# Kernel tuning notes

Measured on AMD Instinct MI355X. Metric: run time of the kernel, lower is better.

Reference implementation:

```python
import jax, jax.numpy as jnp
import numpy as np

EMB = 768
HEADS = 12
B, N = 32, 1024


def setup_inputs() -> dict:
    key = jax.random.key(0)
    ks = jax.random.split(key, 7)
    s = 1.0 / np.sqrt(EMB)
    return {
        "x": jax.random.normal(ks[0], (B, N, EMB), dtype=jnp.float32),
        "Wq": jax.random.normal(ks[1], (EMB, EMB), dtype=jnp.float32) * s,
        "bq": jnp.zeros((EMB,), dtype=jnp.float32),
        "Wk": jax.random.normal(ks[2], (EMB, EMB), dtype=jnp.float32) * s,
        "bk": jnp.zeros((EMB,), dtype=jnp.float32),
        "Wv": jax.random.normal(ks[3], (EMB, EMB), dtype=jnp.float32) * s,
        "bv": jnp.zeros((EMB,), dtype=jnp.float32),
    }


def reference(x, Wq, bq, Wk, bk, Wv, bv):
    b, n, _ = x.shape
    h = HEADS
    e = EMB // h  # head dim
    # project and split heads: b n (h e) -> b h n e
    def split(t):
        return t.reshape(b, n, h, e).transpose(0, 2, 1, 3)
    q = split(x @ Wq + bq)
    k = split(x @ Wk + bk)
    v = split(x @ Wv + bv)
    # NOTE: scale is 1/sqrt(num_head), as in the original module
    wei = jnp.einsum('bhie,bhje->bhij', q, k) / jnp.sqrt(jnp.float32(h))
    # NOTE: softmax over dim=2 = query axis i (non-standard)
    wei = jax.nn.softmax(wei, axis=2)
    # dropout is identity in eval mode
    out = jnp.einsum('bhij,bhje->bhie', wei, v)
    return out.transpose(0, 2, 1, 3).reshape(b, n, h * e)
```

## Files before the change

### kernel.cpp

```cpp
#include <hip/hip_runtime.h>

#define EMB 768
#define NH 12
#define HD 64
#define BB 32
#define NN 1024
#define QSCALE 0.41647025f

typedef _Float16 h8 __attribute__((ext_vector_type(8)));
typedef _Float16 h4 __attribute__((ext_vector_type(4)));
typedef _Float16 h2 __attribute__((ext_vector_type(2)));
typedef float f4 __attribute__((ext_vector_type(4)));

static __device__ __forceinline__ f4 mfma16(h8 a, h8 b, f4 c) {
  return __builtin_amdgcn_mfma_f32_16x16x32_f16(a, b, c, 0, 0, 0);
}

static __device__ __forceinline__ h2 cvt_pk(float a, float b) {
  return __builtin_bit_cast(h2, __builtin_amdgcn_cvt_pkrtz(a, b));
}

static __device__ __forceinline__ float exp2a(float x) {
#if __has_builtin(__builtin_amdgcn_exp2f)
  return __builtin_amdgcn_exp2f(x);
#else
  float r;
  asm("v_exp_f32 %0, %1\n\ts_nop 1" : "=v"(r) : "v"(x));
  return r;
#endif
}

static __device__ __forceinline__ void gload16(const _Float16* g, _Float16* lds) {
  __builtin_amdgcn_global_load_lds(
      (const __attribute__((address_space(1))) void*)g,
      (__attribute__((address_space(3))) void*)lds, 16, 0, 0);
}

__global__ __launch_bounds__(256) void k_cvt(const float* __restrict__ X,
                                             _Float16* __restrict__ Xh, int n4) {
  int i = blockIdx.x * 256 + threadIdx.x;
  if (i >= n4) return;
  float4 v = ((const float4*)X)[i];
  h4 o = {(_Float16)v.x, (_Float16)v.y, (_Float16)v.z, (_Float16)v.w};
  ((h4*)Xh)[i] = o;
}

__global__ __launch_bounds__(256) void k_wt(const float* __restrict__ W0,
                                            const float* __restrict__ W1,
                                            const float* __restrict__ W2,
                                            _Float16* __restrict__ Wt) {
  const float* W = blockIdx.z == 0 ? W0 : (blockIdx.z == 1 ? W1 : W2);
  _Float16* dst = Wt + (size_t)blockIdx.z * EMB * EMB;
  __shared__ float tile[64][65];
  const int t = threadIdx.x;
  const int r0 = blockIdx.y * 64, c0 = blockIdx.x * 64;
  const int r = t >> 4, c4 = (t & 15) * 4;
#pragma unroll
  for (int i = 0; i < 4; ++i) {
    const float4 v = *(const float4*)&W[(size_t)(r0 + r + 16 * i) * EMB + c0 + c4];
    tile[r + 16 * i][c4 + 0] = v.x; tile[r + 16 * i][c4 + 1] = v.y;
    tile[r + 16 * i][c4 + 2] = v.z; tile[r + 16 * i][c4 + 3] = v.w;
  }
  __syncthreads();
  const int cc = t >> 2, rr = (t & 3) * 16;
#pragma unroll
  for (int half = 0; half < 2; ++half) {
    h8 o;
#pragma unroll
    for (int j = 0; j < 8; ++j) o[j] = (_Float16)tile[rr + half * 8 + j][cc];
    *(h8*)&dst[(size_t)(c0 + cc) * EMB + r0 + rr + half * 8] = o;
  }
}

__global__ __launch_bounds__(256) void k_projf(const _Float16* __restrict__ Xh,
                                               const _Float16* __restrict__ Wt,
                                               const float* __restrict__ bq,
                                               const float* __restrict__ bk,
                                               const float* __restrict__ bv,
                                               _Float16* __restrict__ Qw,
                                               _Float16* __restrict__ Kw,
                                               _Float16* __restrict__ Vtmp) {
  __shared__ _Float16 As[2][128 * 64];
  __shared__ _Float16 Bs[2][128 * 64];
  const int t = threadIdx.x;
  const int w = t >> 6, l = t & 63;
  const int wm = w >> 1, wn = w & 1;
  const int p = l & 15, g = l >> 4;
  const int by = blockIdx.x;
  const int m0 = blockIdx.y * 128;
  const int n0 = by * 128;

  f4 acc[4][4];
#pragma unroll
  for (int mf = 0; mf < 4; ++mf)
#pragma unroll
    for (int nf = 0; nf < 4; ++nf) acc[mf][nf] = f4{0.f, 0.f, 0.f, 0.f};

  const int lrow = l >> 3, lch = (l & 7) ^ (l >> 3);

#define STAGE(buf, k0)                                                            \
  {                                                                               \
    _Float16* ab = &As[buf][0];                                                   \
    _Float16* bb = &Bs[buf][0];                                                   \
    _Pragma("unroll") for (int i = 0; i < 4; ++i) {                               \
      const int seg = (w << 2) | i;                                               \
      const int grow = (seg << 3) | lrow;                                         \
      gload16(Xh + (size_t)(m0 + grow) * EMB + (k0) + lch * 8, ab + seg * 512);   \
      gload16(Wt + (size_t)(n0 + grow) * EMB + (k0) + lch * 8, bb + seg * 512);   \
    }                                                                             \
  }

  STAGE(0, 0)
  __syncthreads();

  int cur = 0;
  for (int kt = 0; kt < 12; ++kt) {
    if (kt + 1 < 12) STAGE(cur ^ 1, (kt + 1) * 64)
    const char* asb = (const char*)&As[cur][0];
    const char* bsb = (const char*)&Bs[cur][0];
#pragma unroll
    for (int ks = 0; ks < 2; ++ks) {
      h8 af[4], bf[4];
#pragma unroll
      for (int mf = 0; mf < 4; ++mf)
        af[mf] = *(const h8*)(asb + ((wm * 64 + mf * 16 + p) << 7) +
                              ((((ks << 2) | g) ^ (p & 7)) << 4));
#pragma unroll
      for (int nf = 0; nf < 4; ++nf)
        bf[nf] = *(const h8*)(bsb + ((wn * 64 + nf * 16 + p) << 7) +
                              ((((ks << 2) | g) ^ (p & 7)) << 4));
#pragma unroll
      for (int mf = 0; mf < 4; ++mf)
#pragma unroll
        for (int nf = 0; nf < 4; ++nf) acc[mf][nf] = mfma16(af[mf], bf[nf], acc[mf][nf]);
    }
    __syncthreads();
    cur ^= 1;
  }
#undef STAGE

  const int z = by / 6;
  const int nl0 = (by % 6) * 128;
  const float* bias = z == 0 ? bq : (z == 1 ? bk : bv);
  _Float16* Outz = z == 0 ? Qw : (z == 1 ? Kw : Vtmp);
  const float scale = z == 0 ? QSCALE : 1.0f;
#pragma unroll
  for (int nf = 0; nf < 4; ++nf) {
    const int C = nl0 + wn * 64 + nf * 16 + p;
    const float bvv = bias[C];
    const int h = C >> 6, e = C & 63;
#pragma unroll
    for (int mf = 0; mf < 4; ++mf) {
#pragma unroll
      for (int r = 0; r < 4; ++r) {
        const int R = m0 + wm * 64 + mf * 16 + g * 4 + r;
        const int b = R >> 10, tok = R & 1023;
        Outz[((size_t)(b * NH + h) * NN + tok) * HD + e] = (_Float16)((acc[mf][nf][r] + bvv) * scale);
      }
    }
  }
}

__global__ __launch_bounds__(256) void k_stats(const _Float16* __restrict__ Q,
                                               const _Float16* __restrict__ K,
                                               const _Float16* __restrict__ Vtmp,
                                               float* __restrict__ MT,
                                               _Float16* __restrict__ Vt) {
  const int bh = blockIdx.x * 48 + (blockIdx.y >> 3);
  const int jt = blockIdx.y & 7;
  const int j0 = jt * 128;
  __shared__ __align__(16) char SMEM[35080];
  _Float16* Ks = (_Float16*)SMEM;
  _Float16* Qs = (_Float16*)(SMEM + 16384);
  float* Lj    = (float*)(SMEM + 32768);
  float* reds  = (float*)(SMEM + 33280);
  float* MsShp = (float*)(SMEM + 34312);
  _Float16 (*Vtile)[72] = (_Float16(*)[72])SMEM;
  const _Float16* Qb = Q + (size_t)bh * NN * HD;
  const _Float16* Kb = K + (size_t)bh * NN * HD;
  const int t = threadIdx.x, w = t >> 6, l = t & 63;
  const int wi = w >> 1, wj = w & 1;
  const int p = l & 15, g = l >> 4;
  const int lrow = l >> 3, lch = (l & 7) ^ (l >> 3);

#pragma unroll
  for (int i = 0; i < 4; ++i) {
    const int seg = (w << 2) | i;
    const int grow = (seg << 3) | lrow;
    gload16(Kb + (size_t)(j0 + grow) * HD + lch * 8, Ks + seg * 512);
  }
  if (t < 128) Lj[t] = 0.f;
  __syncthreads();

  const char* ksb = (const char*)Ks;
  const char* qsb = (const char*)Qs;
  for (int i0 = 0; i0 < NN; i0 += 128) {
#pragma unroll
    for (int i = 0; i < 4; ++i) {
      const int seg = (w << 2) | i;
      const int grow = (seg << 3) | lrow;
      gload16(Qb + (size_t)(i0 + grow) * HD + lch * 8, Qs + seg * 512);
    }
    __syncthreads();
    f4 s[4][4];
#pragma unroll
    for (int mf = 0; mf < 4; ++mf)
#pragma unroll
      for (int nf = 0; nf < 4; ++nf) s[mf][nf] = f4{0.f, 0.f, 0.f, 0.f};
#pragma unroll
    for (int ks = 0; ks < 2; ++ks) {
      h8 af[4], bf[4];
#pragma unroll
      for (int mf = 0; mf < 4; ++mf)
        af[mf] = *(const h8*)(qsb + ((wi * 64 + mf * 16 + p) << 7) + ((((ks << 2) | g) ^ (p & 7)) << 4));
#pragma unroll
      for (int nf = 0; nf < 4; ++nf)
        bf[nf] = *(const h8*)(ksb + ((wj * 64 + nf * 16 + p) << 7) + ((((ks << 2) | g) ^ (p & 7)) << 4));
#pragma unroll
      for (int mf = 0; mf < 4; ++mf)
#pragma unroll
        for (int nf = 0; nf < 4; ++nf) s[mf][nf] = mfma16(af[mf], bf[nf], s[mf][nf]);
    }
#pragma unroll
    for (int nf = 0; nf < 4; ++nf) {
      float cs = 0.f;
#pragma unroll
      for (int mf = 0; mf < 4; ++mf)
#pragma unroll
        for (int r = 0; r < 4; ++r) cs += exp2a(s[mf][nf][r]);
      cs += __shfl_xor(cs, 16);
      cs += __shfl_xor(cs, 32);
      if (l < 16) reds[wi * 128 + wj * 64 + nf * 16 + l] = cs;
    }
    __syncthreads();
    if (t < 128) Lj[t] += reds[t] + reds[128 + t];
    __syncthreads();
  }
  if (w == 0) {
    float mv = fmaxf(Lj[l], Lj[l + 64]);
#pragma unroll
    for (int d = 32; d; d >>= 1) mv = fmaxf(mv, __shfl_xor(mv, d));
    if (l == 0) { MsShp[0] = __log2f(mv); MT[bh * 8 + jt] = MsShp[0]; }
  }
  __syncthreads();
  const float rmsc = exp2a(MsShp[0]);

  const _Float16* Vb = Vtmp + (size_t)bh * NN * HD;
  _Float16* Vo = Vt + (size_t)bh * HD * NN;
  const int jr = t >> 3, c8 = (t & 7) * 8;
#pragma unroll
  for (int half = 0; half < 2; ++half) {
#pragma unroll
    for (int i = 0; i < 2; ++i) {
      const int jl = half * 64 + jr + 32 * i;
      const float inv = rmsc / Lj[jl];
      h8 v = *(const h8*)&Vb[(size_t)(j0 + jl) * HD + c8];
      h8 o;
#pragma unroll
      for (int j = 0; j < 8; ++j) o[j] = (_Float16)((float)v[j] * inv);
      *(h8*)&Vtile[jr + 32 * i][c8] = o;
    }
    __syncthreads();
#pragma unroll
    for (int i = 0; i < 2; ++i) {
      h8 o;
#pragma unroll
      for (int j = 0; j < 8; ++j) o[j] = Vtile[c8 + j][jr + 32 * i];
      *(h8*)&Vo[(size_t)(jr + 32 * i) * NN + j0 + half * 64 + c8] = o;
    }
    __syncthreads();
  }
}

__global__ __launch_bounds__(256) void k_out(const _Float16* __restrict__ Q,
                                             const _Float16* __restrict__ K,
                                             const _Float16* __restrict__ Vt,
                                             const float* __restrict__ MT,
                                             float* __restrict__ Out) {
  const int bh = blockIdx.x * 48 + (blockIdx.y >> 2);
  const int i0 = (blockIdx.y & 3) * 256;
  const int b = bh / NH, h = bh % NH;
  __shared__ _Float16 Ks[2][32][64];
  __shared__ _Float16 Vts[2][64][32];
  __shared__ _Float16 Ps[4][2][32][32];
  const _Float16* Qb = Q + (size_t)bh * NN * HD;
  const _Float16* Kb = K + (size_t)bh * NN * HD;
  const _Float16* Vb = Vt + (size_t)bh * HD * NN;
  const int t = threadIdx.x, w = t >> 6, l = t & 63;
  const int p = l & 15, g = l >> 4;
  char* psb[2] = {(char*)&Ps[w][0][0][0], (char*)&Ps[w][1][0][0]};

  h8 bq[2][2][2];
#pragma unroll
  for (int it = 0; it < 2; ++it)
#pragma unroll
    for (int f = 0; f < 2; ++f)
#pragma unroll
      for (int ks = 0; ks < 2; ++ks)
        bq[it][f][ks] = *(const h8*)&Qb[(size_t)(i0 + it * 128 + w * 32 + f * 16 + p) * HD + ks * 32 + g * 8];

  f4 oacc[2][4][2];
#pragma unroll
  for (int it = 0; it < 2; ++it)
#pragma unroll
    for (int ef = 0; ef < 4; ++ef)
#pragma unroll
      for (int f = 0; f < 2; ++f) oacc[it][ef][f] = f4{0.f, 0.f, 0.f, 0.f};

  const int kr = t >> 3, kc = t & 7;
  const int vr = t >> 2, vc = t & 3;

  h8 kreg = *(const h8*)&Kb[(size_t)kr * HD + kc * 8];
  h8 vreg = *(const h8*)&Vb[(size_t)vr * NN + vc * 8];
  *(h8*)((char*)&Ks[0][0][0] + (kr << 7) + ((kc ^ (kr & 7)) << 4)) = kreg;
  *(h8*)((char*)&Vts[0][0][0] + (vr << 6) + ((vc ^ ((vr >> 1) & 3)) << 4)) = vreg;

  for (int jt4 = 0; jt4 < 8; ++jt4) {
    const float Mstar = MT[bh * 8 + jt4];
#pragma unroll
    for (int u = 0; u < 4; ++u) {
      const int jt = jt4 * 4 + u;
      const int cur = u & 1;
      char* ksb = (char*)&Ks[cur][0][0];
      char* vsb = (char*)&Vts[cur][0][0];
      __syncthreads();
      if (jt + 1 < 32) {
        const int j0n = (jt + 1) * 32;
        kreg = *(const h8*)&Kb[(size_t)(j0n + kr) * HD + kc * 8];
        vreg = *(const h8*)&Vb[(size_t)vr * NN + j0n + vc * 8];
      }

      h8 ak[2][2], av[4];
#pragma unroll
      for (int ks = 0; ks < 2; ++ks)
#pragma unroll
        for (int jf = 0; jf < 2; ++jf)
          ak[ks][jf] = *(const h8*)(ksb + ((jf * 16 + p) << 7) + ((((ks << 2) | g) ^ (p & 7)) << 4));
#pragma unroll
      for (int ef = 0; ef < 4; ++ef)
        av[ef] = *(const h8*)(vsb + ((ef * 16 + p) << 6) + ((g ^ ((p >> 1) & 3)) << 4));

#pragma unroll
      for (int it = 0; it < 2; ++it) {
        f4 s[2][2];
#pragma unroll
        for (int f = 0; f < 2; ++f)
#pragma unroll
          for (int jf = 0; jf < 2; ++jf) s[f][jf] = f4{-Mstar, -Mstar, -Mstar, -Mstar};
#pragma unroll
        for (int ks = 0; ks < 2; ++ks)
#pragma unroll
          for (int f = 0; f < 2; ++f)
#pragma unroll
            for (int jf = 0; jf < 2; ++jf) s[f][jf] = mfma16(ak[ks][jf], bq[it][f][ks], s[f][jf]);
#pragma unroll
        for (int f = 0; f < 2; ++f)
#pragma unroll
          for (int jf = 0; jf < 2; ++jf) {
            const f4 sv = s[f][jf];
            h2 lo = cvt_pk(exp2a(sv[0]), exp2a(sv[1]));
            h2 hi = cvt_pk(exp2a(sv[2]), exp2a(sv[3]));
            h4 pw; pw[0] = lo[0]; pw[1] = lo[1]; pw[2] = hi[0]; pw[3] = hi[1];
            *(h4*)(psb[it] + ((f * 16 + p) << 6) +
                   (((2 * jf + (g >> 1)) ^ ((p >> 1) & 3)) << 4) + ((g & 1) << 3)) = pw;
          }
      }
      asm volatile("s_waitcnt lgkmcnt(0)" ::: "memory");
      __builtin_amdgcn_sched_barrier(0);

#pragma unroll
      for (int it = 0; it < 2; ++it) {
        h8 bp[2];
#pragma unroll
        for (int f = 0; f < 2; ++f)
          bp[f] = *(const h8*)(psb[it] + ((f * 16 + p) << 6) + ((g ^ ((p >> 1) & 3)) << 4));
#pragma unroll
        for (int ef = 0; ef < 4; ++ef)
#pragma unroll
          for (int f = 0; f < 2; ++f) oacc[it][ef][f] = mfma16(av[ef], bp[f], oacc[it][ef][f]);
      }

      if (jt + 1 < 32) {
        *(h8*)((char*)&Ks[cur ^ 1][0][0] + (kr << 7) + ((kc ^ (kr & 7)) << 4)) = kreg;
        *(h8*)((char*)&Vts[cur ^ 1][0][0] + (vr << 6) + ((vc ^ ((vr >> 1) & 3)) << 4)) = vreg;
      }
    }
  }

#pragma unroll
  for (int it = 0; it < 2; ++it) {
#pragma unroll
    for (int f = 0; f < 2; ++f) {
      const int i = i0 + it * 128 + w * 32 + f * 16 + p;
#pragma unroll
      for (int ef = 0; ef < 4; ++ef) {
        float4 o4 = {oacc[it][ef][f][0], oacc[it][ef][f][1], oacc[it][ef][f][2], oacc[it][ef][f][3]};
        *(float4*)&Out[((size_t)b * NN + i) * EMB + h * HD + ef * 16 + 4 * g] = o4;
      }
    }
  }
}

extern "C" void kernel_launch(void* const* d_in, const int* in_sizes, int n_in,
                              void* d_out, int out_size, void* d_ws, size_t ws_size,
                              hipStream_t stream) {
  const float* X  = (const float*)d_in[0];
  const float* Wq = (const float*)d_in[1];
  const float* bq = (const float*)d_in[2];
  const float* Wk = (const float*)d_in[3];
  const float* bk = (const float*)d_in[4];
  const float* Wv = (const float*)d_in[5];
  const float* bv = (const float*)d_in[6];

  char* ws = (char*)d_ws;
  _Float16* Qw = (_Float16*)(ws);
  _Float16* Kw = (_Float16*)(ws + 50331648);
  _Float16* Vt = (_Float16*)(ws + 100663296);
  _Float16* Wt = (_Float16*)(ws + 150994944);
  float* MT    = (float*)(ws + 154533888);

  _Float16* Xh   = (_Float16*)d_out;
  _Float16* Vtmp = (_Float16*)((char*)d_out + 50331648);
  float* Out = (float*)d_out;

  k_cvt<<<dim3(6291456 / 256), 256, 0, stream>>>(X, Xh, 6291456);
  k_wt<<<dim3(12, 12, 3), 256, 0, stream>>>(Wq, Wk, Wv, Wt);
  k_projf<<<dim3(18, 256), 256, 0, stream>>>(Xh, Wt, bq, bk, bv, Qw, Kw, Vtmp);
  k_stats<<<dim3(8, 384), 256, 0, stream>>>(Qw, Kw, Vtmp, MT, Vt);
  k_out<<<dim3(8, 192), 256, 0, stream>>>(Qw, Kw, Vt, MT, Out);
}
```

Before: 386.4 us.

## Load projection weights directly from global, remap blocks per XCD, double-buffer Q in stats

In the projection GEMM, the weight tile is no longer staged through shared memory. Each wave reads its B fragments directly from global memory, which halves LDS use and may raise occupancy, at the cost of uncoalesced global loads that depend on L2 hits. The grid is flattened and remapped so that each XCD works on a contiguous range of M tiles, which should improve L2 reuse of X and W. The stats kernel double-buffers the Q tile so the next tile's load overlaps the current compute, at the cost of more shared memory per block.

```diff
diff --git a/kernel.cpp b/kernel.cpp
--- a/kernel.cpp
+++ b/kernel.cpp
@@ -81,13 +81,15 @@
                                                _Float16* __restrict__ Kw,
                                                _Float16* __restrict__ Vtmp) {
   __shared__ _Float16 As[2][128 * 64];
-  __shared__ _Float16 Bs[2][128 * 64];
   const int t = threadIdx.x;
   const int w = t >> 6, l = t & 63;
   const int wm = w >> 1, wn = w & 1;
   const int p = l & 15, g = l >> 4;
-  const int by = blockIdx.x;
-  const int m0 = blockIdx.y * 128;
+  const int bid = blockIdx.x;
+  const int xcd = bid & 7, idx = bid >> 3;
+  const int mi = idx / 18;
+  const int by = idx - mi * 18;
+  const int m0 = (xcd * 32 + mi) * 128;
   const int n0 = by * 128;
 
   f4 acc[4][4];
@@ -98,38 +100,37 @@
 
   const int lrow = l >> 3, lch = (l & 7) ^ (l >> 3);
 
-#define STAGE(buf, k0)                                                            \
+#define STAGEA(buf, k0)                                                           \
   {                                                                               \
     _Float16* ab = &As[buf][0];                                                   \
-    _Float16* bb = &Bs[buf][0];                                                   \
     _Pragma("unroll") for (int i = 0; i < 4; ++i) {                               \
       const int seg = (w << 2) | i;                                               \
       const int grow = (seg << 3) | lrow;                                         \
       gload16(Xh + (size_t)(m0 + grow) * EMB + (k0) + lch * 8, ab + seg * 512);   \
-      gload16(Wt + (size_t)(n0 + grow) * EMB + (k0) + lch * 8, bb + seg * 512);   \
     }                                                                             \
   }
 
-  STAGE(0, 0)
+  STAGEA(0, 0)
   __syncthreads();
+
+  const _Float16* Bb = Wt + (size_t)(n0 + wn * 64 + p) * EMB + g * 8;
 
   int cur = 0;
   for (int kt = 0; kt < 12; ++kt) {
-    if (kt + 1 < 12) STAGE(cur ^ 1, (kt + 1) * 64)
+    const int k0 = kt * 64;
+    if (kt + 1 < 12) STAGEA(cur ^ 1, k0 + 64)
     const char* asb = (const char*)&As[cur][0];
-    const char* bsb = (const char*)&Bs[cur][0];
 #pragma unroll
     for (int ks = 0; ks < 2; ++ks) {
       h8 af[4], bf[4];
+#pragma unroll
+      for (int nf = 0; nf < 4; ++nf)
+        bf[nf] = *(const h8*)&Bb[(size_t)(nf * 16) * EMB + k0 + ks * 32];
 #pragma unroll
       for (int mf = 0; mf < 4; ++mf)
         af[mf] = *(const h8*)(asb + ((wm * 64 + mf * 16 + p) << 7) +
                               ((((ks << 2) | g) ^ (p & 7)) << 4));
 #pragma unroll
-      for (int nf = 0; nf < 4; ++nf)
-        bf[nf] = *(const h8*)(bsb + ((wn * 64 + nf * 16 + p) << 7) +
-                              ((((ks << 2) | g) ^ (p & 7)) << 4));
-#pragma unroll
       for (int mf = 0; mf < 4; ++mf)
 #pragma unroll
         for (int nf = 0; nf < 4; ++nf) acc[mf][nf] = mfma16(af[mf], bf[nf], acc[mf][nf]);
@@ -137,7 +138,7 @@
     __syncthreads();
     cur ^= 1;
   }
-#undef STAGE
+#undef STAGEA
 
   const int z = by / 6;
   const int nl0 = (by % 6) * 128;
@@ -169,13 +170,15 @@
   const int bh = blockIdx.x * 48 + (blockIdx.y >> 3);
   const int jt = blockIdx.y & 7;
   const int j0 = jt * 128;
-  __shared__ __align__(16) char SMEM[35080];
-  _Float16* Ks = (_Float16*)SMEM;
-  _Float16* Qs = (_Float16*)(SMEM + 16384);
-  float* Lj    = (float*)(SMEM + 32768);
-  float* reds  = (float*)(SMEM + 33280);
-  float* MsShp = (float*)(SMEM + 34312);
+  __shared__ __align__(16) char SMEM[50704];
+  _Float16* Ks   = (_Float16*)SMEM;
+  _Float16* Qs0  = (_Float16*)(SMEM + 16384);
+  _Float16* Qs1  = (_Float16*)(SMEM + 32768);
+  float* Lj      = (float*)(SMEM + 49152);
+  float* reds    = (float*)(SMEM + 49664);
+  float* MsShp   = (float*)(SMEM + 50688);
   _Float16 (*Vtile)[72] = (_Float16(*)[72])SMEM;
+  _Float16* qsBuf[2] = {Qs0, Qs1};
   const _Float16* Qb = Q + (size_t)bh * NN * HD;
   const _Float16* Kb = K + (size_t)bh * NN * HD;
   const int t = threadIdx.x, w = t >> 6, l = t & 63;
@@ -183,25 +186,30 @@
   const int p = l & 15, g = l >> 4;
   const int lrow = l >> 3, lch = (l & 7) ^ (l >> 3);
 
+#define STAGEQ(dst, i0v)                                                          \
+  {                                                                               \
+    _Pragma("unroll") for (int i = 0; i < 4; ++i) {                               \
+      const int seg = (w << 2) | i;                                               \
+      const int grow = (seg << 3) | lrow;                                         \
+      gload16(Qb + (size_t)((i0v) + grow) * HD + lch * 8, (dst) + seg * 512);     \
+    }                                                                             \
+  }
+
 #pragma unroll
   for (int i = 0; i < 4; ++i) {
     const int seg = (w << 2) | i;
     const int grow = (seg << 3) | lrow;
     gload16(Kb + (size_t)(j0 + grow) * HD + lch * 8, Ks + seg * 512);
   }
+  STAGEQ(Qs0, 0)
   if (t < 128) Lj[t] = 0.f;
   __syncthreads();
 
   const char* ksb = (const char*)Ks;
-  const char* qsb = (const char*)Qs;
+  int cur = 0;
   for (int i0 = 0; i0 < NN; i0 += 128) {
-#pragma unroll
-    for (int i = 0; i < 4; ++i) {
-      const int seg = (w << 2) | i;
-      const int grow = (seg << 3) | lrow;
-      gload16(Qb + (size_t)(i0 + grow) * HD + lch * 8, Qs + seg * 512);
-    }
-    __syncthreads();
+    if (i0 + 128 < NN) STAGEQ(qsBuf[cur ^ 1], i0 + 128)
+    const char* qsb = (const char*)qsBuf[cur];
     f4 s[4][4];
 #pragma unroll
     for (int mf = 0; mf < 4; ++mf)
@@ -235,7 +243,9 @@
     __syncthreads();
     if (t < 128) Lj[t] += reds[t] + reds[128 + t];
     __syncthreads();
-  }
+    cur ^= 1;
+  }
+#undef STAGEQ
   if (w == 0) {
     float mv = fmaxf(Lj[l], Lj[l + 64]);
 #pragma unroll
@@ -425,7 +435,7 @@
 
   k_cvt<<<dim3(6291456 / 256), 256, 0, stream>>>(X, Xh, 6291456);
   k_wt<<<dim3(12, 12, 3), 256, 0, stream>>>(Wq, Wk, Wv, Wt);
-  k_projf<<<dim3(18, 256), 256, 0, stream>>>(Xh, Wt, bq, bk, bv, Qw, Kw, Vtmp);
+  k_projf<<<dim3(4608), 256, 0, stream>>>(Xh, Wt, bq, bk, bv, Qw, Kw, Vtmp);
   k_stats<<<dim3(8, 384), 256, 0, stream>>>(Qw, Kw, Vtmp, MT, Vt);
   k_out<<<dim3(8, 192), 256, 0, stream>>>(Qw, Kw, Vt, MT, Out);
 }
```

Result: slower. 476.2 us (+23.2%).
